# Optimization experiments

Measured on AMD Instinct MI355X. Metric: run time of the kernel, lower is better.

Reference implementation:

```python
import jax, jax.numpy as jnp
import numpy as np

B, N, D, H, DH, M = 4, 4096, 1024, 16, 64, 256
EPS = 1e-4


def softmax_kernel(data, P, is_query):
    # data: [b,h,n,dh], P: [m,dh]  (FAVOR+ positive softmax features)
    dn = data.shape[-1] ** -0.25
    ratio = P.shape[0] ** -0.5
    dd = jnp.einsum('bhnd,md->bhnm', dn * data, P)
    diag = (jnp.sum(data * data, axis=-1) * 0.5 * dn * dn)[..., None]  # [b,h,n,1]
    if is_query:
        mx = jnp.max(dd, axis=-1, keepdims=True)  # per-query max
    else:
        mx = jnp.max(dd)  # global max (as in torch source)
    return ratio * (jnp.exp(dd - diag - mx) + EPS)


def setup_inputs() -> dict:
    key = jax.random.key(0)
    ks = jax.random.split(key, 6)
    s = 1.0 / np.sqrt(D).astype(np.float32)
    x = jax.random.normal(ks[0], (B, N, D), jnp.float32)
    Wq = jax.random.normal(ks[1], (D, H * DH), jnp.float32) * s
    Wk = jax.random.normal(ks[2], (D, H * DH), jnp.float32) * s
    Wv = jax.random.normal(ks[3], (D, H * DH), jnp.float32) * s
    Wo = jax.random.normal(ks[4], (H * DH, D), jnp.float32) * s
    bo = jnp.zeros((D,), jnp.float32)
    P = jax.random.normal(ks[5], (M, DH), jnp.float32)  # gaussian (orthogonal) projection
    return {'x': x, 'Wq': Wq, 'Wk': Wk, 'Wv': Wv, 'Wo': Wo, 'bo': bo, 'P': P}


def reference(x, Wq, Wk, Wv, Wo, bo, P):
    b, n, _ = x.shape
    # qkv projections, split heads: b n (h d) -> b h n d
    def proj(W):
        return (x @ W).reshape(b, n, H, DH).transpose(0, 2, 1, 3)
    q, k, v = proj(Wq), proj(Wk), proj(Wv)
    qp = softmax_kernel(q, P, is_query=True)   # [b,h,n,m]
    kp = softmax_kernel(k, P, is_query=False)  # [b,h,n,m]
    # linear attention (Performer)
    k_cumsum = kp.sum(axis=-2)                                   # [b,h,m]
    D_inv = 1.0 / jnp.einsum('bhnm,bhm->bhn', qp, k_cumsum)      # [b,h,n]
    ctx = jnp.einsum('bhnm,bhne->bhme', kp, v)                   # [b,h,m,dh]
    out = jnp.einsum('bhme,bhnm,bhn->bhne', ctx, qp, D_inv)      # [b,h,n,dh]
    out = out.transpose(0, 2, 1, 3).reshape(b, n, H * DH)
    return out @ Wo + bo
```

## Files before the change

kernel.cpp:

```cpp
#include <hip/hip_runtime.h>
#include <math.h>

#define NB 4
#define NSEQ 4096
#define DM 1024
#define NHEAD 16
#define DHD 64
#define MF 256
#define ROWS 16384

#define DN 0.35355339059327373f
#define RATIO 0.0625f
#define HALF_DN2 0.0625f
#define EPSF 1.0e-4f

typedef __attribute__((ext_vector_type(4))) float f32x4;
typedef __attribute__((ext_vector_type(8))) short short8;
typedef __attribute__((ext_vector_type(4))) short short4v;
typedef __attribute__((ext_vector_type(8))) __bf16 bf16x8;
typedef unsigned short ushort_t;

__device__ __forceinline__ unsigned short f2bf(float f) {
  unsigned int u = __builtin_bit_cast(unsigned int, f);
  u += 0x7FFFu + ((u >> 16) & 1u);
  return (unsigned short)(u >> 16);
}
__device__ __forceinline__ float bf2f(unsigned short h) {
  unsigned int u = ((unsigned int)h) << 16;
  return __builtin_bit_cast(float, u);
}

__device__ __forceinline__ f32x4 mfma16(short8 a, short8 b, f32x4 c) {
  return __builtin_amdgcn_mfma_f32_16x16x32_bf16(
      __builtin_bit_cast(bf16x8, a), __builtin_bit_cast(bf16x8, b), c, 0, 0, 0);
}

__device__ __forceinline__ f32x4 mfma16x16(short4v a, short4v b, f32x4 c) {
#if __has_builtin(__builtin_amdgcn_mfma_f32_16x16x16bf16_1k)
  return __builtin_amdgcn_mfma_f32_16x16x16bf16_1k(a, b, c, 0, 0, 0);
#elif __has_builtin(__builtin_amdgcn_mfma_f32_16x16x16_bf16)
  typedef __attribute__((ext_vector_type(4))) __bf16 bf16x4;
  return __builtin_amdgcn_mfma_f32_16x16x16_bf16(
      __builtin_bit_cast(bf16x4, a), __builtin_bit_cast(bf16x4, b), c, 0, 0, 0);
#else
  asm volatile("s_nop 1\n\t"
               "v_mfma_f32_16x16x16_bf16 %0, %1, %2, %0\n\t"
               "s_nop 7"
               : "+v"(c) : "v"(a), "v"(b));
  return c;
#endif
}

__device__ __forceinline__ void glds16(const void* g, void* l) {
  __builtin_amdgcn_global_load_lds(
      (const __attribute__((address_space(1))) unsigned int*)g,
      (__attribute__((address_space(3))) unsigned int*)l, 16, 0, 0);
}

__global__ __launch_bounds__(256) void wtrans(const float* __restrict__ W,
                                              ushort_t* __restrict__ Wt)
{
  __shared__ float ts[64][68];
  const int tid = threadIdx.x;
  const int k0 = blockIdx.y * 64, n0 = blockIdx.x * 64;
  const int r = tid >> 4, c4 = (tid & 15) * 4;
  #pragma unroll
  for (int i = 0; i < 4; ++i) {
    float4 v = *(const float4*)&W[(size_t)(k0 + r + i * 16) * DM + n0 + c4];
    *(float4*)&ts[r + i * 16][c4] = v;
  }
  __syncthreads();
  #pragma unroll
  for (int i = 0; i < 4; ++i) {
    const int n = r + i * 16;
    ushort4 o;
    o.x = f2bf(ts[c4 + 0][n]); o.y = f2bf(ts[c4 + 1][n]);
    o.z = f2bf(ts[c4 + 2][n]); o.w = f2bf(ts[c4 + 3][n]);
    *(ushort4*)&Wt[(size_t)(n0 + n) * DM + k0 + c4] = o;
  }
}

__global__ __launch_bounds__(256) void psplit(const float* __restrict__ P,
                                              ushort_t* __restrict__ PHI,
                                              ushort_t* __restrict__ PLO)
{
  const int i = blockIdx.x * 256 + threadIdx.x;
  const float v = P[i];
  const unsigned short h = f2bf(v);
  PHI[i] = h;
  PLO[i] = f2bf(v - bf2f(h));
}

__global__ __launch_bounds__(256) void xconv(const float* __restrict__ x,
                                             ushort_t* __restrict__ xb)
{
  const size_t i = ((size_t)blockIdx.x * 256 + threadIdx.x) * 8;
  const float4 a = *(const float4*)&x[i];
  const float4 c = *(const float4*)&x[i + 4];
  short8 o;
  o[0] = f2bf(a.x); o[1] = f2bf(a.y); o[2] = f2bf(a.z); o[3] = f2bf(a.w);
  o[4] = f2bf(c.x); o[5] = f2bf(c.y); o[6] = f2bf(c.z); o[7] = f2bf(c.w);
  *(short8*)&xb[i] = o;
}

template<bool AF32, int EPI>
__global__ __launch_bounds__(256) void gemm_k(const float* __restrict__ Af,
                                              const ushort_t* __restrict__ Ab,
                                              const ushort_t* __restrict__ Bt,
                                              const float* __restrict__ bias,
                                              float* __restrict__ C,
                                              ushort_t* __restrict__ VT,
                                              ushort_t* __restrict__ OH,
                                              ushort_t* __restrict__ OL)
{
  constexpr int K = DM, N = DM;
  __shared__ ushort_t As[128 * 32];
  __shared__ ushort_t Bs[128 * 32];

  const int tid = threadIdx.x;
  const int l = tid & 63, w = tid >> 6;
  const int ll = l & 15, lh = l >> 4;
  const int wr = w >> 1, wc = w & 1;

  const int bid = blockIdx.x;
  const int swz = (bid & 7) * ((int)gridDim.x >> 3) + (bid >> 3);
  const int bm = swz >> 3, bn = swz & 7;
  const int row0 = bm * 128, col0 = bn * 128;

  const int pb0 = w * 128 + l, pb1 = pb0 + 64;
  const int brow0 = pb0 >> 2, bkq0 = (pb0 & 3) ^ ((brow0 >> 1) & 3);
  const int brow1 = pb1 >> 2, bkq1 = (pb1 & 3) ^ ((brow1 >> 1) & 3);
  const ushort_t* bsrc0 = Bt + (size_t)(col0 + brow0) * K + bkq0 * 8;
  const ushort_t* bsrc1 = Bt + (size_t)(col0 + brow1) * K + bkq1 * 8;
  ushort_t* bdst0 = &Bs[(size_t)(w * 128) * 8];
  ushort_t* bdst1 = &Bs[(size_t)(w * 128 + 64) * 8];

  const int pa0 = tid, pa1 = tid + 256;
  const int arow0 = pa0 >> 2, akq0 = (pa0 & 3) ^ ((arow0 >> 1) & 3);
  const int arow1 = pa1 >> 2, akq1 = (pa1 & 3) ^ ((arow1 >> 1) & 3);
  const float* afs0 = nullptr; const float* afs1 = nullptr;
  const ushort_t* abs0_ = nullptr; const ushort_t* abs1_ = nullptr;
  if constexpr (AF32) {
    afs0 = Af + (size_t)(row0 + arow0) * K + akq0 * 8;
    afs1 = Af + (size_t)(row0 + arow1) * K + akq1 * 8;
  } else {
    abs0_ = Ab + (size_t)(row0 + brow0) * K + bkq0 * 8;
    abs1_ = Ab + (size_t)(row0 + brow1) * K + bkq1 * 8;
  }

  int aoff[4], boff[4];
  #pragma unroll
  for (int mt = 0; mt < 4; ++mt) {
    const int r = wr * 64 + mt * 16 + ll;
    aoff[mt] = (r * 4 + (lh ^ ((r >> 1) & 3))) * 8;
  }
  #pragma unroll
  for (int nt = 0; nt < 4; ++nt) {
    const int r = wc * 64 + nt * 16 + ll;
    boff[nt] = (r * 4 + (lh ^ ((r >> 1) & 3))) * 8;
  }

  f32x4 acc[4][4];
  #pragma unroll
  for (int i = 0; i < 4; ++i)
    #pragma unroll
    for (int j = 0; j < 4; ++j) acc[i][j] = (f32x4){0.f, 0.f, 0.f, 0.f};

  for (int k0 = 0; k0 < K; k0 += 32) {
    __syncthreads();
    if constexpr (AF32) {
      const float4 u0 = *(const float4*)(afs0 + k0);
      const float4 u1 = *(const float4*)(afs0 + k0 + 4);
      const float4 v0 = *(const float4*)(afs1 + k0);
      const float4 v1 = *(const float4*)(afs1 + k0 + 4);
      short8 s0, s1;
      s0[0] = f2bf(u0.x); s0[1] = f2bf(u0.y); s0[2] = f2bf(u0.z); s0[3] = f2bf(u0.w);
      s0[4] = f2bf(u1.x); s0[5] = f2bf(u1.y); s0[6] = f2bf(u1.z); s0[7] = f2bf(u1.w);
      s1[0] = f2bf(v0.x); s1[1] = f2bf(v0.y); s1[2] = f2bf(v0.z); s1[3] = f2bf(v0.w);
      s1[4] = f2bf(v1.x); s1[5] = f2bf(v1.y); s1[6] = f2bf(v1.z); s1[7] = f2bf(v1.w);
      *(short8*)&As[(size_t)pa0 * 8] = s0;
      *(short8*)&As[(size_t)pa1 * 8] = s1;
    } else {
      glds16(abs0_ + k0, &As[(size_t)(w * 128) * 8]);
      glds16(abs1_ + k0, &As[(size_t)(w * 128 + 64) * 8]);
    }
    glds16(bsrc0 + k0, bdst0);
    glds16(bsrc1 + k0, bdst1);
    __syncthreads();

    short8 av[4], bv[4];
    #pragma unroll
    for (int mt = 0; mt < 4; ++mt) av[mt] = *(const short8*)&As[aoff[mt]];
    #pragma unroll
    for (int nt = 0; nt < 4; ++nt) bv[nt] = *(const short8*)&Bs[boff[nt]];
    #pragma unroll
    for (int mt = 0; mt < 4; ++mt)
      #pragma unroll
      for (int nt = 0; nt < 4; ++nt)
        acc[mt][nt] = mfma16(av[mt], bv[nt], acc[mt][nt]);
  }

  if constexpr (EPI <= 1) {
    #pragma unroll
    for (int mt = 0; mt < 4; ++mt) {
      #pragma unroll
      for (int nt = 0; nt < 4; ++nt) {
        const int row = row0 + wr * 64 + mt * 16 + lh * 4;
        const int col = col0 + wc * 64 + nt * 16 + ll;
        const float bv_ = (EPI == 1) ? bias[col] : 0.f;
        #pragma unroll
        for (int j = 0; j < 4; ++j)
          C[(size_t)(row + j) * N + col] = acc[mt][nt][j] + bv_;
      }
    }
  } else if constexpr (EPI == 2) {
    #pragma unroll
    for (int mt = 0; mt < 4; ++mt) {
      #pragma unroll
      for (int nt = 0; nt < 4; ++nt) {
        const int rg = row0 + wr * 64 + mt * 16 + lh * 4;
        const int cg = col0 + wc * 64 + nt * 16 + ll;
        const int b = rg >> 12, n = rg & 4095;
        const int h = cg >> 6, dh = cg & 63;
        ushort4 o;
        o.x = f2bf(acc[mt][nt][0]); o.y = f2bf(acc[mt][nt][1]);
        o.z = f2bf(acc[mt][nt][2]); o.w = f2bf(acc[mt][nt][3]);
        *(ushort4*)&VT[(((size_t)b * 16 + h) * 64 + dh) * 4096 + n] = o;
      }
    }
  } else {
    #pragma unroll
    for (int mt = 0; mt < 4; ++mt) {
      #pragma unroll
      for (int nt = 0; nt < 4; ++nt) {
        const int row = row0 + wr * 64 + mt * 16 + lh * 4;
        const int col = col0 + wc * 64 + nt * 16 + ll;
        #pragma unroll
        for (int j = 0; j < 4; ++j) {
          const float v = acc[mt][nt][j];
          const unsigned short hh = f2bf(v);
          OH[(size_t)(row + j) * N + col] = hh;
          OL[(size_t)(row + j) * N + col] = f2bf(v - bf2f(hh));
        }
      }
    }
  }
}

__global__ __launch_bounds__(256) void kmax3(const ushort_t* __restrict__ KHI,
                                             const ushort_t* __restrict__ KLO,
                                             const ushort_t* __restrict__ PHI,
                                             const ushort_t* __restrict__ PLO,
                                             unsigned* __restrict__ mxp)
{
  const int tid = threadIdx.x;
  const int l = tid & 63, mg = tid >> 6;
  const int ll = l & 15, lh = l >> 4;
  const int bh = blockIdx.x >> 4, ck = blockIdx.x & 15;
  const int b = bh >> 4, h = bh & 15;

  short8 pfh[4][2], pfl[4][2];
  #pragma unroll
  for (int mt = 0; mt < 4; ++mt)
    #pragma unroll
    for (int ks = 0; ks < 2; ++ks) {
      const size_t off = (size_t)(mg * 64 + mt * 16 + ll) * 64 + ks * 32 + lh * 8;
      pfh[mt][ks] = *(const short8*)&PHI[off];
      pfl[mt][ks] = *(const short8*)&PLO[off];
    }

  float vmax = -3.0e38f;
  for (int it = 0; it < 16; ++it) {
    const int nb = ck * 256 + it * 16;
    const size_t off = ((size_t)(b * NSEQ + nb + ll)) * DM + h * DHD + lh * 8;
    short8 kh0 = *(const short8*)&KHI[off];
    short8 kh1 = *(const short8*)&KHI[off + 32];
    short8 kl0 = *(const short8*)&KLO[off];
    short8 kl1 = *(const short8*)&KLO[off + 32];
    #pragma unroll
    for (int mt = 0; mt < 4; ++mt) {
      f32x4 acc = (f32x4){0.f, 0.f, 0.f, 0.f};
      acc = mfma16(kh0, pfh[mt][0], acc); acc = mfma16(kh1, pfh[mt][1], acc);
      acc = mfma16(kh0, pfl[mt][0], acc); acc = mfma16(kh1, pfl[mt][1], acc);
      acc = mfma16(kl0, pfh[mt][0], acc); acc = mfma16(kl1, pfh[mt][1], acc);
      vmax = fmaxf(vmax, fmaxf(fmaxf(acc[0], acc[1]), fmaxf(acc[2], acc[3])));
    }
  }
  vmax *= DN;
  #pragma unroll
  for (int off = 1; off < 64; off <<= 1) vmax = fmaxf(vmax, __shfl_xor(vmax, off, 64));
  if (l == 0) atomicMax(mxp, __float_as_uint(vmax));
}

__global__ __launch_bounds__(256) void kside4(const ushort_t* __restrict__ KHI,
                                              const ushort_t* __restrict__ KLO,
                                              const ushort_t* __restrict__ VT,
                                              const ushort_t* __restrict__ PHI,
                                              const ushort_t* __restrict__ PLO,
                                              const unsigned* __restrict__ mxp,
                                              float* __restrict__ ctx,
                                              float* __restrict__ kcs)
{
  const int tid = threadIdx.x;
  const int l = tid & 63, mg = tid >> 6;
  const int ll = l & 15, lh = l >> 4;
  const int bh = blockIdx.x >> 4, ck = blockIdx.x & 15;
  const int b = bh >> 4, h = bh & 15;

  short8 pfh[4][2], pfl[4][2];
  #pragma unroll
  for (int mt = 0; mt < 4; ++mt)
    #pragma unroll
    for (int ks = 0; ks < 2; ++ks) {
      const size_t off = (size_t)(mg * 64 + mt * 16 + ll) * 64 + ks * 32 + lh * 8;
      pfh[mt][ks] = *(const short8*)&PHI[off];
      pfl[mt][ks] = *(const short8*)&PLO[off];
    }
  const float mx = __uint_as_float(*mxp);

  f32x4 apv[4][4];
  #pragma unroll
  for (int i = 0; i < 4; ++i)
    #pragma unroll
    for (int j = 0; j < 4; ++j) apv[i][j] = (f32x4){0.f, 0.f, 0.f, 0.f};
  float kcp[4] = {0.f, 0.f, 0.f, 0.f};

  for (int it = 0; it < 16; ++it) {
    const int nb = ck * 256 + it * 16;
    const size_t off = ((size_t)(b * NSEQ + nb + ll)) * DM + h * DHD + lh * 8;
    short8 kh0 = *(const short8*)&KHI[off];
    short8 kh1 = *(const short8*)&KHI[off + 32];
    short8 kl0 = *(const short8*)&KLO[off];
    short8 kl1 = *(const short8*)&KLO[off + 32];

    float ssq = 0.f;
    #pragma unroll
    for (int e = 0; e < 8; ++e) {
      const float a0 = bf2f((ushort_t)kh0[e]) + bf2f((ushort_t)kl0[e]);
      const float a1 = bf2f((ushort_t)kh1[e]) + bf2f((ushort_t)kl1[e]);
      ssq += a0 * a0 + a1 * a1;
    }
    ssq += __shfl_xor(ssq, 16, 64);
    ssq += __shfl_xor(ssq, 32, 64);
    const float dgl = HALF_DN2 * ssq;
    float dgv[4];
    #pragma unroll
    for (int jr = 0; jr < 4; ++jr)
      dgv[jr] = __shfl(dgl, ((l >> 4) << 2) + jr, 64);

    short4v qa[4];
    #pragma unroll
    for (int mt = 0; mt < 4; ++mt) {
      f32x4 acc = (f32x4){0.f, 0.f, 0.f, 0.f};
      acc = mfma16(kh0, pfh[mt][0], acc); acc = mfma16(kh1, pfh[mt][1], acc);
      acc = mfma16(kh0, pfl[mt][0], acc); acc = mfma16(kh1, pfl[mt][1], acc);
      acc = mfma16(kl0, pfh[mt][0], acc); acc = mfma16(kl1, pfh[mt][1], acc);
      short4v o; float s = 0.f;
      #pragma unroll
      for (int jr = 0; jr < 4; ++jr) {
        const float kv = RATIO * (__expf(acc[jr] * DN - dgv[jr] - mx) + EPSF);
        const ushort_t ub = f2bf(kv);
        o[jr] = (short)ub;
        s += bf2f(ub);
      }
      qa[mt] = o;
      kcp[mt] += s;
    }
    #pragma unroll
    for (int dt = 0; dt < 4; ++dt) {
      const short4v vf = *(const short4v*)&VT[((size_t)bh * 64 + dt * 16 + ll) * NSEQ + nb + lh * 4];
      #pragma unroll
      for (int mt = 0; mt < 4; ++mt)
        apv[mt][dt] = mfma16x16(qa[mt], vf, apv[mt][dt]);
    }
  }

  #pragma unroll
  for (int mt = 0; mt < 4; ++mt) {
    float s = kcp[mt];
    s += __shfl_xor(s, 16, 64);
    s += __shfl_xor(s, 32, 64);
    if (lh == 0) atomicAdd(&kcs[bh * MF + mg * 64 + mt * 16 + ll], s);
  }
  #pragma unroll
  for (int mt = 0; mt < 4; ++mt)
    #pragma unroll
    for (int dt = 0; dt < 4; ++dt)
      #pragma unroll
      for (int jr = 0; jr < 4; ++jr) {
        const int m = mg * 64 + mt * 16 + lh * 4 + jr;
        const int dh = dt * 16 + ll;
        atomicAdd(&ctx[((size_t)bh * MF + m) * DHD + dh], apv[mt][dt][jr]);
      }
}

__global__ __launch_bounds__(256) void ctx2bf(const float* __restrict__ ctx,
                                              ushort_t* __restrict__ CTH,
                                              ushort_t* __restrict__ CTL)
{
  __shared__ float ts[64][68];
  const int tid = threadIdx.x;
  const int bh = blockIdx.x >> 2, mc = blockIdx.x & 3;
  const int r = tid >> 4, c4 = (tid & 15) * 4;
  #pragma unroll
  for (int i = 0; i < 4; ++i) {
    const int m = mc * 64 + r + i * 16;
    *(float4*)&ts[r + i * 16][c4] = *(const float4*)&ctx[((size_t)bh * MF + m) * DHD + c4];
  }
  __syncthreads();
  #pragma unroll
  for (int i = 0; i < 4; ++i) {
    const int dh = r + i * 16;
    ushort4 oh, ol;
    #pragma unroll
    for (int k = 0; k < 4; ++k) {
      const float v = ts[c4 + k][dh];
      const unsigned short hh = f2bf(v);
      ((unsigned short*)&oh)[k] = hh;
      ((unsigned short*)&ol)[k] = f2bf(v - bf2f(hh));
    }
    const size_t o = ((size_t)bh * 64 + dh) * MF + mc * 64 + c4;
    *(ushort4*)&CTH[o] = oh;
    *(ushort4*)&CTL[o] = ol;
  }
}

__global__ __launch_bounds__(512, 2) void qside5(const ushort_t* __restrict__ QHI,
                                                 const ushort_t* __restrict__ QLO,
                                                 const ushort_t* __restrict__ PHI,
                                                 const ushort_t* __restrict__ PLO,
                                                 const float* __restrict__ kcs,
                                                 const ushort_t* __restrict__ CTH,
                                                 const ushort_t* __restrict__ CTL,
                                                 ushort_t* __restrict__ attb)
{
  extern __shared__ ushort_t lds[];
  ushort_t* pst = lds;
  ushort_t* ctf = lds + 32768;
  ushort_t* kcf = lds + 65536;

  const int tid = threadIdx.x;
  const int l = tid & 63, w = tid >> 6;
  const int ll = l & 15, lh = l >> 4;
  const int bh = blockIdx.x >> 4, qt = blockIdx.x & 15;
  const int b = bh >> 4, h = bh & 15;

  #pragma unroll
  for (int i = 0; i < 8; ++i) {
    const int f = tid + i * 512;
    const int fl = f & 63, r = f >> 6;
    const int p = r & 1, ks = (r >> 1) & 1, mt = r >> 2;
    const ushort_t* src = (p ? PLO : PHI) + (mt * 16 + (fl & 15)) * 64 + ks * 32 + (fl >> 4) * 8;
    *(short8*)&pst[f * 8] = *(const short8*)src;
  }
  #pragma unroll
  for (int i = 0; i < 16; ++i) {
    const int g = tid + i * 512;
    const int gl = g & 63, r = g >> 6;
    const int dt = r & 3, r2 = r >> 2, mt = r2 & 15, p = r2 >> 4;
    const ushort_t* src = (p ? CTL : CTH) +
        ((size_t)bh * 64 + dt * 16 + (gl & 15)) * MF + mt * 16 + (gl >> 4) * 4;
    *(ushort4*)&ctf[g * 4] = *(const ushort4*)src;
  }
  #pragma unroll
  for (int i = 0; i < 2; ++i) {
    const int u = tid + i * 512;
    const int ul = u & 63, mt = u >> 6;
    const int cll = ul & 15, clh = ul >> 4;
    ushort4 o = make_ushort4(0, 0, 0, 0);
    if (cll < 2) {
      #pragma unroll
      for (int e = 0; e < 4; ++e) {
        const float kv = kcs[bh * MF + mt * 16 + clh * 4 + e];
        const unsigned short hi = f2bf(kv);
        ((ushort_t*)&o)[e] = (cll == 0) ? hi : f2bf(kv - bf2f(hi));
      }
    }
    *(ushort4*)&kcf[u * 4] = o;
  }
  __syncthreads();

  const int rowb0 = b * NSEQ + qt * 256 + w * 32;

  short8 qh0[2], ql0[2], qh1[2], ql1[2];
  #pragma unroll
  for (int ks = 0; ks < 2; ++ks) {
    const size_t off = (size_t)(rowb0 + ll) * DM + h * DHD + ks * 32 + lh * 8;
    qh0[ks] = *(const short8*)&QHI[off];
    ql0[ks] = *(const short8*)&QLO[off];
    qh1[ks] = *(const short8*)&QHI[off + (size_t)16 * DM];
    ql1[ks] = *(const short8*)&QLO[off + (size_t)16 * DM];
  }
  float ssq0 = 0.f, ssq1 = 0.f;
  #pragma unroll
  for (int ks = 0; ks < 2; ++ks)
    #pragma unroll
    for (int e = 0; e < 8; ++e) {
      const float a0 = bf2f((ushort_t)qh0[ks][e]) + bf2f((ushort_t)ql0[ks][e]);
      const float a1 = bf2f((ushort_t)qh1[ks][e]) + bf2f((ushort_t)ql1[ks][e]);
      ssq0 += a0 * a0; ssq1 += a1 * a1;
    }
  ssq0 += __shfl_xor(ssq0, 16, 64); ssq0 += __shfl_xor(ssq0, 32, 64);
  ssq1 += __shfl_xor(ssq1, 16, 64); ssq1 += __shfl_xor(ssq1, 32, 64);
  const float dg0 = HALF_DN2 * ssq0, dg1 = HALF_DN2 * ssq1;

  f32x4 dd0[16], dd1[16];
  #pragma unroll
  for (int mt = 0; mt < 16; ++mt) {
    const short8 ph0 = *(const short8*)&pst[((mt * 2 + 0) * 2 + 0) * 512 + l * 8];
    const short8 ph1 = *(const short8*)&pst[((mt * 2 + 1) * 2 + 0) * 512 + l * 8];
    const short8 pl0 = *(const short8*)&pst[((mt * 2 + 0) * 2 + 1) * 512 + l * 8];
    const short8 pl1 = *(const short8*)&pst[((mt * 2 + 1) * 2 + 1) * 512 + l * 8];
    f32x4 a0 = (f32x4){0.f, 0.f, 0.f, 0.f};
    f32x4 a1 = (f32x4){0.f, 0.f, 0.f, 0.f};
    a0 = mfma16(ph0, qh0[0], a0); a0 = mfma16(ph1, qh0[1], a0);
    a0 = mfma16(ph0, ql0[0], a0); a0 = mfma16(ph1, ql0[1], a0);
    a0 = mfma16(pl0, qh0[0], a0); a0 = mfma16(pl1, qh0[1], a0);
    a1 = mfma16(ph0, qh1[0], a1); a1 = mfma16(ph1, qh1[1], a1);
    a1 = mfma16(ph0, ql1[0], a1); a1 = mfma16(ph1, ql1[1], a1);
    a1 = mfma16(pl0, qh1[0], a1); a1 = mfma16(pl1, qh1[1], a1);
    dd0[mt] = a0; dd1[mt] = a1;
  }

  float rm0 = -3.0e38f, rm1 = -3.0e38f;
  #pragma unroll
  for (int mt = 0; mt < 16; ++mt) {
    rm0 = fmaxf(rm0, fmaxf(fmaxf(dd0[mt][0], dd0[mt][1]), fmaxf(dd0[mt][2], dd0[mt][3])));
    rm1 = fmaxf(rm1, fmaxf(fmaxf(dd1[mt][0], dd1[mt][1]), fmaxf(dd1[mt][2], dd1[mt][3])));
  }
  rm0 = fmaxf(rm0, __shfl_xor(rm0, 16, 64)); rm0 = fmaxf(rm0, __shfl_xor(rm0, 32, 64));
  rm1 = fmaxf(rm1, __shfl_xor(rm1, 16, 64)); rm1 = fmaxf(rm1, __shfl_xor(rm1, 32, 64));
  rm0 *= DN; rm1 *= DN;

  short4v qp0[16], qp1[16];
  #pragma unroll
  for (int mt = 0; mt < 16; ++mt) {
    short4v o0, o1;
    #pragma unroll
    for (int jr = 0; jr < 4; ++jr) {
      o0[jr] = (short)f2bf(RATIO * (__expf(dd0[mt][jr] * DN - dg0 - rm0) + EPSF));
      o1[jr] = (short)f2bf(RATIO * (__expf(dd1[mt][jr] * DN - dg1 - rm1) + EPSF));
    }
    qp0[mt] = o0; qp1[mt] = o1;
  }

  f32x4 av0[4], av1[4];
  #pragma unroll
  for (int dt = 0; dt < 4; ++dt) {
    av0[dt] = (f32x4){0.f, 0.f, 0.f, 0.f};
    av1[dt] = (f32x4){0.f, 0.f, 0.f, 0.f};
  }
  f32x4 aK0 = (f32x4){0.f, 0.f, 0.f, 0.f};
  f32x4 aK1 = (f32x4){0.f, 0.f, 0.f, 0.f};
  #pragma unroll
  for (int mt = 0; mt < 16; ++mt) {
    const short4v kcv = *(const short4v*)&kcf[mt * 256 + l * 4];
    aK0 = mfma16x16(qp0[mt], kcv, aK0);
    aK1 = mfma16x16(qp1[mt], kcv, aK1);
    #pragma unroll
    for (int dt = 0; dt < 4; ++dt) {
      const short4v ch = *(const short4v*)&ctf[((0 * 16 + mt) * 4 + dt) * 256 + l * 4];
      const short4v cl = *(const short4v*)&ctf[((16 + mt) * 4 + dt) * 256 + l * 4];
      av0[dt] = mfma16x16(qp0[mt], ch, av0[dt]);
      av0[dt] = mfma16x16(qp0[mt], cl, av0[dt]);
      av1[dt] = mfma16x16(qp1[mt], ch, av1[dt]);
      av1[dt] = mfma16x16(qp1[mt], cl, av1[dt]);
    }
  }

  float di0[4], di1[4];
  #pragma unroll
  for (int jr = 0; jr < 4; ++jr) {
    const float h0 = __shfl(aK0[jr], (l & 48), 64);
    const float l0 = __shfl(aK0[jr], (l & 48) | 1, 64);
    const float h1 = __shfl(aK1[jr], (l & 48), 64);
    const float l1 = __shfl(aK1[jr], (l & 48) | 1, 64);
    di0[jr] = 1.0f / (h0 + l0);
    di1[jr] = 1.0f / (h1 + l1);
  }

  #pragma unroll
  for (int dt = 0; dt < 4; ++dt)
    #pragma unroll
    for (int jr = 0; jr < 4; ++jr) {
      const int col = h * DHD + dt * 16 + ll;
      attb[(size_t)(rowb0 + lh * 4 + jr) * DM + col] = f2bf(av0[dt][jr] * di0[jr]);
      attb[(size_t)(rowb0 + 16 + lh * 4 + jr) * DM + col] = f2bf(av1[dt][jr] * di1[jr]);
    }
}

extern "C" void kernel_launch(void* const* d_in, const int* in_sizes, int n_in,
                              void* d_out, int out_size, void* d_ws, size_t ws_size,
                              hipStream_t stream)
{
  const float* x  = (const float*)d_in[0];
  const float* Wq = (const float*)d_in[1];
  const float* Wk = (const float*)d_in[2];
  const float* Wv = (const float*)d_in[3];
  const float* Wo = (const float*)d_in[4];
  const float* bo = (const float*)d_in[5];
  const float* P  = (const float*)d_in[6];
  float* out = (float*)d_out;

  char* wp = (char*)d_ws;
  ushort_t* QHI = (ushort_t*)(wp + 0);
  ushort_t* QLO = (ushort_t*)(wp + 33554432);
  ushort_t* KHI = (ushort_t*)(wp + 67108864);
  ushort_t* KLO = (ushort_t*)(wp + 100663296);
  ushort_t* VT  = (ushort_t*)(wp + 134217728);
  ushort_t* Wqt = (ushort_t*)(wp + 167772160);
  ushort_t* Wkt = (ushort_t*)(wp + 169869312);
  ushort_t* Wvt = (ushort_t*)(wp + 171966464);
  ushort_t* Wot = (ushort_t*)(wp + 174063616);
  ushort_t* PHI = (ushort_t*)(wp + 176160768);
  ushort_t* PLO = (ushort_t*)(wp + 176193536);
  float*    CTX = (float*)(wp + 176226304);
  float*    KCS = (float*)(wp + 180420608);
  unsigned* MX  = (unsigned*)(wp + 180486144);
  ushort_t* CTH = (ushort_t*)(wp + 180486400);
  ushort_t* CTL = (ushort_t*)(wp + 182583552);
  ushort_t* XB  = (ushort_t*)(wp + 184680704);
  ushort_t* ATTB = KHI;

  const bool useXB = ws_size >= 218235136ull;

  dim3 tg(16, 16);
  wtrans<<<tg, 256, 0, stream>>>(Wq, Wqt);
  wtrans<<<tg, 256, 0, stream>>>(Wk, Wkt);
  wtrans<<<tg, 256, 0, stream>>>(Wv, Wvt);
  wtrans<<<tg, 256, 0, stream>>>(Wo, Wot);
  psplit<<<64, 256, 0, stream>>>(P, PHI, PLO);

  if (useXB) {
    xconv<<<8192, 256, 0, stream>>>(x, XB);
    gemm_k<false, 3><<<1024, 256, 0, stream>>>(nullptr, XB, Wqt, nullptr, nullptr, nullptr, QHI, QLO);
    gemm_k<false, 3><<<1024, 256, 0, stream>>>(nullptr, XB, Wkt, nullptr, nullptr, nullptr, KHI, KLO);
    gemm_k<false, 2><<<1024, 256, 0, stream>>>(nullptr, XB, Wvt, nullptr, nullptr, VT, nullptr, nullptr);
  } else {
    gemm_k<true, 3><<<1024, 256, 0, stream>>>(x, nullptr, Wqt, nullptr, nullptr, nullptr, QHI, QLO);
    gemm_k<true, 3><<<1024, 256, 0, stream>>>(x, nullptr, Wkt, nullptr, nullptr, nullptr, KHI, KLO);
    gemm_k<true, 2><<<1024, 256, 0, stream>>>(x, nullptr, Wvt, nullptr, nullptr, VT, nullptr, nullptr);
  }

  hipMemsetAsync(CTX, 0, 4194304 + 65536 + 256, stream);

  kmax3<<<1024, 256, 0, stream>>>(KHI, KLO, PHI, PLO, MX);
  kside4<<<1024, 256, 0, stream>>>(KHI, KLO, VT, PHI, PLO, MX, CTX, KCS);
  ctx2bf<<<256, 256, 0, stream>>>(CTX, CTH, CTL);
  qside5<<<1024, 512, 139264, stream>>>(QHI, QLO, PHI, PLO, KCS, CTH, CTL, ATTB);

  gemm_k<false, 1><<<1024, 256, 0, stream>>>(nullptr, ATTB, Wot, bo, out, nullptr, nullptr, nullptr);
}
```

Baseline: 534.5 us.

## Fuse key max pass into key-side accumulation with online rescaling

Replaces the separate key-max kernel and atomic-based key-side kernel with one pass that keeps a running per-wave max with deferred rescaling. It writes per-chunk partial context and key sums that a combine kernel later rescales by the global max, and folds the epsilon term in through a V column sum. The projection GEMM epilogue now computes the squared-norm diagonal and writes interleaved hi/lo Q/K rows. Scratch buffers live in the output buffer so the bf16 x path is always taken. This removes one full read of K, the fp32 atomics and the extra memset, at the cost of larger partial buffers and a more complex combine step.

```diff
diff --git a/kernel.cpp b/kernel.cpp
--- a/kernel.cpp
+++ b/kernel.cpp
@@ -13,6 +13,7 @@
 #define RATIO 0.0625f
 #define HALF_DN2 0.0625f
 #define EPSF 1.0e-4f
+#define THR_DEFER 4.0f
 
 typedef __attribute__((ext_vector_type(4))) float f32x4;
 typedef __attribute__((ext_vector_type(8))) short short8;
@@ -103,15 +104,14 @@
   *(short8*)&xb[i] = o;
 }
 
-template<bool AF32, int EPI>
-__global__ __launch_bounds__(256) void gemm_k(const float* __restrict__ Af,
-                                              const ushort_t* __restrict__ Ab,
+template<int EPI>
+__global__ __launch_bounds__(256) void gemm_k(const ushort_t* __restrict__ Ab,
                                               const ushort_t* __restrict__ Bt,
                                               const float* __restrict__ bias,
                                               float* __restrict__ C,
                                               ushort_t* __restrict__ VT,
-                                              ushort_t* __restrict__ OH,
-                                              ushort_t* __restrict__ OL)
+                                              ushort_t* __restrict__ OHL,
+                                              float* __restrict__ DIAG)
 {
   constexpr int K = DM, N = DM;
   __shared__ ushort_t As[128 * 32];
@@ -135,18 +135,8 @@
   ushort_t* bdst0 = &Bs[(size_t)(w * 128) * 8];
   ushort_t* bdst1 = &Bs[(size_t)(w * 128 + 64) * 8];
 
-  const int pa0 = tid, pa1 = tid + 256;
-  const int arow0 = pa0 >> 2, akq0 = (pa0 & 3) ^ ((arow0 >> 1) & 3);
-  const int arow1 = pa1 >> 2, akq1 = (pa1 & 3) ^ ((arow1 >> 1) & 3);
-  const float* afs0 = nullptr; const float* afs1 = nullptr;
-  const ushort_t* abs0_ = nullptr; const ushort_t* abs1_ = nullptr;
-  if constexpr (AF32) {
-    afs0 = Af + (size_t)(row0 + arow0) * K + akq0 * 8;
-    afs1 = Af + (size_t)(row0 + arow1) * K + akq1 * 8;
-  } else {
-    abs0_ = Ab + (size_t)(row0 + brow0) * K + bkq0 * 8;
-    abs1_ = Ab + (size_t)(row0 + brow1) * K + bkq1 * 8;
-  }
+  const ushort_t* asrc0 = Ab + (size_t)(row0 + brow0) * K + bkq0 * 8;
+  const ushort_t* asrc1 = Ab + (size_t)(row0 + brow1) * K + bkq1 * 8;
 
   int aoff[4], boff[4];
   #pragma unroll
@@ -168,22 +158,8 @@
 
   for (int k0 = 0; k0 < K; k0 += 32) {
     __syncthreads();
-    if constexpr (AF32) {
-      const float4 u0 = *(const float4*)(afs0 + k0);
-      const float4 u1 = *(const float4*)(afs0 + k0 + 4);
-      const float4 v0 = *(const float4*)(afs1 + k0);
-      const float4 v1 = *(const float4*)(afs1 + k0 + 4);
-      short8 s0, s1;
-      s0[0] = f2bf(u0.x); s0[1] = f2bf(u0.y); s0[2] = f2bf(u0.z); s0[3] = f2bf(u0.w);
-      s0[4] = f2bf(u1.x); s0[5] = f2bf(u1.y); s0[6] = f2bf(u1.z); s0[7] = f2bf(u1.w);
-      s1[0] = f2bf(v0.x); s1[1] = f2bf(v0.y); s1[2] = f2bf(v0.z); s1[3] = f2bf(v0.w);
-      s1[4] = f2bf(v1.x); s1[5] = f2bf(v1.y); s1[6] = f2bf(v1.z); s1[7] = f2bf(v1.w);
-      *(short8*)&As[(size_t)pa0 * 8] = s0;
-      *(short8*)&As[(size_t)pa1 * 8] = s1;
-    } else {
-      glds16(abs0_ + k0, &As[(size_t)(w * 128) * 8]);
-      glds16(abs1_ + k0, &As[(size_t)(w * 128 + 64) * 8]);
-    }
+    glds16(asrc0 + k0, &As[(size_t)(w * 128) * 8]);
+    glds16(asrc1 + k0, &As[(size_t)(w * 128 + 64) * 8]);
     glds16(bsrc0 + k0, bdst0);
     glds16(bsrc1 + k0, bdst1);
     __syncthreads();
@@ -200,14 +176,14 @@
         acc[mt][nt] = mfma16(av[mt], bv[nt], acc[mt][nt]);
   }
 
-  if constexpr (EPI <= 1) {
+  if constexpr (EPI == 1) {
     #pragma unroll
     for (int mt = 0; mt < 4; ++mt) {
       #pragma unroll
       for (int nt = 0; nt < 4; ++nt) {
         const int row = row0 + wr * 64 + mt * 16 + lh * 4;
         const int col = col0 + wc * 64 + nt * 16 + ll;
-        const float bv_ = (EPI == 1) ? bias[col] : 0.f;
+        const float bv_ = bias[col];
         #pragma unroll
         for (int j = 0; j < 4; ++j)
           C[(size_t)(row + j) * N + col] = acc[mt][nt][j] + bv_;
@@ -229,34 +205,54 @@
       }
     }
   } else {
+    const int hglob = (col0 >> 6) + wc;
     #pragma unroll
     for (int mt = 0; mt < 4; ++mt) {
+      float rssq[4] = {0.f, 0.f, 0.f, 0.f};
       #pragma unroll
       for (int nt = 0; nt < 4; ++nt) {
         const int row = row0 + wr * 64 + mt * 16 + lh * 4;
-        const int col = col0 + wc * 64 + nt * 16 + ll;
+        const int e = nt * 16 + ll;
         #pragma unroll
         for (int j = 0; j < 4; ++j) {
           const float v = acc[mt][nt][j];
+          rssq[j] += v * v;
           const unsigned short hh = f2bf(v);
-          OH[(size_t)(row + j) * N + col] = hh;
-          OL[(size_t)(row + j) * N + col] = f2bf(v - bf2f(hh));
+          const size_t base = ((size_t)(row + j) * 16 + hglob) * 128 + e;
+          OHL[base] = hh;
+          OHL[base + 64] = f2bf(v - bf2f(hh));
         }
       }
-    }
-  }
-}
-
-__global__ __launch_bounds__(256) void kmax3(const ushort_t* __restrict__ KHI,
-                                             const ushort_t* __restrict__ KLO,
-                                             const ushort_t* __restrict__ PHI,
-                                             const ushort_t* __restrict__ PLO,
-                                             unsigned* __restrict__ mxp)
+      #pragma unroll
+      for (int j = 0; j < 4; ++j) {
+        float s = rssq[j];
+        s += __shfl_xor(s, 1, 64); s += __shfl_xor(s, 2, 64);
+        s += __shfl_xor(s, 4, 64); s += __shfl_xor(s, 8, 64);
+        if (ll == 0) {
+          const int row = row0 + wr * 64 + mt * 16 + lh * 4 + j;
+          DIAG[(((row >> 12) * 16 + hglob) << 12) + (row & 4095)] = HALF_DN2 * s;
+        }
+      }
+    }
+  }
+}
+
+__global__ __launch_bounds__(256) void kside5(const ushort_t* __restrict__ KHL,
+                                              const ushort_t* __restrict__ VT,
+                                              const ushort_t* __restrict__ PHI,
+                                              const ushort_t* __restrict__ PLO,
+                                              const float* __restrict__ DIAGK,
+                                              float* __restrict__ partC,
+                                              float* __restrict__ partK,
+                                              float* __restrict__ mw,
+                                              float* __restrict__ vsum,
+                                              unsigned* __restrict__ mxp)
 {
   const int tid = threadIdx.x;
   const int l = tid & 63, mg = tid >> 6;
   const int ll = l & 15, lh = l >> 4;
-  const int bh = blockIdx.x >> 4, ck = blockIdx.x & 15;
+  const int blk = blockIdx.x;
+  const int bh = blk >> 3, ck = blk & 7;
   const int b = bh >> 4, h = bh & 15;
 
   short8 pfh[4][2], pfl[4][2];
@@ -269,110 +265,104 @@
       pfl[mt][ks] = *(const short8*)&PLO[off];
     }
 
-  float vmax = -3.0e38f;
-  for (int it = 0; it < 16; ++it) {
-    const int nb = ck * 256 + it * 16;
-    const size_t off = ((size_t)(b * NSEQ + nb + ll)) * DM + h * DHD + lh * 8;
-    short8 kh0 = *(const short8*)&KHI[off];
-    short8 kh1 = *(const short8*)&KHI[off + 32];
-    short8 kl0 = *(const short8*)&KLO[off];
-    short8 kl1 = *(const short8*)&KLO[off + 32];
+  f32x4 apv[4][4];
+  #pragma unroll
+  for (int i = 0; i < 4; ++i)
+    #pragma unroll
+    for (int j = 0; j < 4; ++j) apv[i][j] = (f32x4){0.f, 0.f, 0.f, 0.f};
+  float kcp[4] = {0.f, 0.f, 0.f, 0.f};
+  float vs[4] = {0.f, 0.f, 0.f, 0.f};
+  float m_run = -1.0e30f, tmax = -1.0e30f;
+
+  const int n0 = ck * 512;
+  const ushort_t* krow = KHL + ((size_t)(b * NSEQ + n0 + ll) * 16 + h) * 128 + lh * 8;
+  const ushort_t* vrow = VT + (size_t)bh * 64 * NSEQ + n0 + lh * 4;
+  const float* drow = DIAGK + bh * 4096 + n0 + lh * 4;
+
+  short8 kh0 = *(const short8*)(krow);
+  short8 kh1 = *(const short8*)(krow + 32);
+  short8 kl0 = *(const short8*)(krow + 64);
+  short8 kl1 = *(const short8*)(krow + 96);
+
+  for (int it = 0; it < 32; ++it) {
+    short8 nh0, nh1, nl0, nl1;
+    if (it < 31) {
+      const ushort_t* kp = krow + (size_t)(it + 1) * 16 * 2048;
+      nh0 = *(const short8*)(kp);
+      nh1 = *(const short8*)(kp + 32);
+      nl0 = *(const short8*)(kp + 64);
+      nl1 = *(const short8*)(kp + 96);
+    }
+    const float4 dg4 = *(const float4*)(drow + it * 16);
+    short4v vf[4];
+    #pragma unroll
+    for (int dt = 0; dt < 4; ++dt)
+      vf[dt] = *(const short4v*)&vrow[(size_t)(dt * 16 + ll) * NSEQ + it * 16];
+
+    f32x4 dda[4];
     #pragma unroll
     for (int mt = 0; mt < 4; ++mt) {
       f32x4 acc = (f32x4){0.f, 0.f, 0.f, 0.f};
       acc = mfma16(kh0, pfh[mt][0], acc); acc = mfma16(kh1, pfh[mt][1], acc);
       acc = mfma16(kh0, pfl[mt][0], acc); acc = mfma16(kh1, pfl[mt][1], acc);
       acc = mfma16(kl0, pfh[mt][0], acc); acc = mfma16(kl1, pfh[mt][1], acc);
-      vmax = fmaxf(vmax, fmaxf(fmaxf(acc[0], acc[1]), fmaxf(acc[2], acc[3])));
-    }
-  }
-  vmax *= DN;
-  #pragma unroll
-  for (int off = 1; off < 64; off <<= 1) vmax = fmaxf(vmax, __shfl_xor(vmax, off, 64));
-  if (l == 0) atomicMax(mxp, __float_as_uint(vmax));
-}
-
-__global__ __launch_bounds__(256) void kside4(const ushort_t* __restrict__ KHI,
-                                              const ushort_t* __restrict__ KLO,
-                                              const ushort_t* __restrict__ VT,
-                                              const ushort_t* __restrict__ PHI,
-                                              const ushort_t* __restrict__ PLO,
-                                              const unsigned* __restrict__ mxp,
-                                              float* __restrict__ ctx,
-                                              float* __restrict__ kcs)
-{
-  const int tid = threadIdx.x;
-  const int l = tid & 63, mg = tid >> 6;
-  const int ll = l & 15, lh = l >> 4;
-  const int bh = blockIdx.x >> 4, ck = blockIdx.x & 15;
-  const int b = bh >> 4, h = bh & 15;
-
-  short8 pfh[4][2], pfl[4][2];
-  #pragma unroll
-  for (int mt = 0; mt < 4; ++mt)
-    #pragma unroll
-    for (int ks = 0; ks < 2; ++ks) {
-      const size_t off = (size_t)(mg * 64 + mt * 16 + ll) * 64 + ks * 32 + lh * 8;
-      pfh[mt][ks] = *(const short8*)&PHI[off];
-      pfl[mt][ks] = *(const short8*)&PLO[off];
-    }
-  const float mx = __uint_as_float(*mxp);
-
-  f32x4 apv[4][4];
-  #pragma unroll
-  for (int i = 0; i < 4; ++i)
-    #pragma unroll
-    for (int j = 0; j < 4; ++j) apv[i][j] = (f32x4){0.f, 0.f, 0.f, 0.f};
-  float kcp[4] = {0.f, 0.f, 0.f, 0.f};
-
-  for (int it = 0; it < 16; ++it) {
-    const int nb = ck * 256 + it * 16;
-    const size_t off = ((size_t)(b * NSEQ + nb + ll)) * DM + h * DHD + lh * 8;
-    short8 kh0 = *(const short8*)&KHI[off];
-    short8 kh1 = *(const short8*)&KHI[off + 32];
-    short8 kl0 = *(const short8*)&KLO[off];
-    short8 kl1 = *(const short8*)&KLO[off + 32];
-
-    float ssq = 0.f;
-    #pragma unroll
-    for (int e = 0; e < 8; ++e) {
-      const float a0 = bf2f((ushort_t)kh0[e]) + bf2f((ushort_t)kl0[e]);
-      const float a1 = bf2f((ushort_t)kh1[e]) + bf2f((ushort_t)kl1[e]);
-      ssq += a0 * a0 + a1 * a1;
-    }
-    ssq += __shfl_xor(ssq, 16, 64);
-    ssq += __shfl_xor(ssq, 32, 64);
-    const float dgl = HALF_DN2 * ssq;
-    float dgv[4];
-    #pragma unroll
-    for (int jr = 0; jr < 4; ++jr)
-      dgv[jr] = __shfl(dgl, ((l >> 4) << 2) + jr, 64);
-
+      #pragma unroll
+      for (int jr = 0; jr < 4; ++jr) acc[jr] *= DN;
+      dda[mt] = acc;
+    }
+
+    float pm = -1.0e30f;
+    #pragma unroll
+    for (int mt = 0; mt < 4; ++mt)
+      #pragma unroll
+      for (int jr = 0; jr < 4; ++jr) pm = fmaxf(pm, dda[mt][jr]);
+    tmax = fmaxf(tmax, pm);
+    if (!__all(pm <= m_run + THR_DEFER)) {
+      float pw = pm;
+      pw = fmaxf(pw, __shfl_xor(pw, 1, 64));  pw = fmaxf(pw, __shfl_xor(pw, 2, 64));
+      pw = fmaxf(pw, __shfl_xor(pw, 4, 64));  pw = fmaxf(pw, __shfl_xor(pw, 8, 64));
+      pw = fmaxf(pw, __shfl_xor(pw, 16, 64)); pw = fmaxf(pw, __shfl_xor(pw, 32, 64));
+      const float sc = __expf(m_run - pw);
+      #pragma unroll
+      for (int mt = 0; mt < 4; ++mt) {
+        kcp[mt] *= sc;
+        #pragma unroll
+        for (int dt = 0; dt < 4; ++dt) apv[mt][dt] *= sc;
+      }
+      m_run = pw;
+    }
+
+    const float dgv[4] = {dg4.x, dg4.y, dg4.z, dg4.w};
     short4v qa[4];
     #pragma unroll
     for (int mt = 0; mt < 4; ++mt) {
-      f32x4 acc = (f32x4){0.f, 0.f, 0.f, 0.f};
-      acc = mfma16(kh0, pfh[mt][0], acc); acc = mfma16(kh1, pfh[mt][1], acc);
-      acc = mfma16(kh0, pfl[mt][0], acc); acc = mfma16(kh1, pfl[mt][1], acc);
-      acc = mfma16(kl0, pfh[mt][0], acc); acc = mfma16(kl1, pfh[mt][1], acc);
-      short4v o; float s = 0.f;
+      short4v o;
+      float s = 0.f;
       #pragma unroll
       for (int jr = 0; jr < 4; ++jr) {
-        const float kv = RATIO * (__expf(acc[jr] * DN - dgv[jr] - mx) + EPSF);
-        const ushort_t ub = f2bf(kv);
+        const float kv = __expf(dda[mt][jr] - dgv[jr] - m_run);
+        const unsigned short ub = f2bf(kv);
         o[jr] = (short)ub;
         s += bf2f(ub);
       }
       qa[mt] = o;
       kcp[mt] += s;
     }
-    #pragma unroll
-    for (int dt = 0; dt < 4; ++dt) {
-      const short4v vf = *(const short4v*)&VT[((size_t)bh * 64 + dt * 16 + ll) * NSEQ + nb + lh * 4];
+
+    if (mg == 0) {
+      #pragma unroll
+      for (int dt = 0; dt < 4; ++dt)
+        #pragma unroll
+        for (int e = 0; e < 4; ++e) vs[dt] += bf2f((ushort_t)vf[dt][e]);
+    }
+
+    #pragma unroll
+    for (int dt = 0; dt < 4; ++dt)
       #pragma unroll
       for (int mt = 0; mt < 4; ++mt)
-        apv[mt][dt] = mfma16x16(qa[mt], vf, apv[mt][dt]);
-    }
+        apv[mt][dt] = mfma16x16(qa[mt], vf[dt], apv[mt][dt]);
+
+    kh0 = nh0; kh1 = nh1; kl0 = nl0; kl1 = nl1;
   }
 
   #pragma unroll
@@ -380,7 +370,7 @@
     float s = kcp[mt];
     s += __shfl_xor(s, 16, 64);
     s += __shfl_xor(s, 32, 64);
-    if (lh == 0) atomicAdd(&kcs[bh * MF + mg * 64 + mt * 16 + ll], s);
+    if (lh == 0) partK[blk * 256 + mg * 64 + mt * 16 + ll] = s;
   }
   #pragma unroll
   for (int mt = 0; mt < 4; ++mt)
@@ -390,22 +380,66 @@
       for (int jr = 0; jr < 4; ++jr) {
         const int m = mg * 64 + mt * 16 + lh * 4 + jr;
         const int dh = dt * 16 + ll;
-        atomicAdd(&ctx[((size_t)bh * MF + m) * DHD + dh], apv[mt][dt][jr]);
-      }
-}
-
-__global__ __launch_bounds__(256) void ctx2bf(const float* __restrict__ ctx,
-                                              ushort_t* __restrict__ CTH,
-                                              ushort_t* __restrict__ CTL)
-{
-  __shared__ float ts[64][68];
+        partC[(size_t)blk * 16384 + (size_t)m * 64 + dh] = apv[mt][dt][jr];
+      }
+  if (mg == 0) {
+    #pragma unroll
+    for (int dt = 0; dt < 4; ++dt) {
+      float s = vs[dt];
+      s += __shfl_xor(s, 16, 64);
+      s += __shfl_xor(s, 32, 64);
+      if (lh == 0) atomicAdd(&vsum[bh * 64 + dt * 16 + ll], s);
+    }
+  }
+  tmax = fmaxf(tmax, __shfl_xor(tmax, 1, 64));  tmax = fmaxf(tmax, __shfl_xor(tmax, 2, 64));
+  tmax = fmaxf(tmax, __shfl_xor(tmax, 4, 64));  tmax = fmaxf(tmax, __shfl_xor(tmax, 8, 64));
+  tmax = fmaxf(tmax, __shfl_xor(tmax, 16, 64)); tmax = fmaxf(tmax, __shfl_xor(tmax, 32, 64));
+  if (l == 0) {
+    atomicMax(mxp, __float_as_uint(tmax));
+    mw[blk * 4 + mg] = m_run;
+  }
+}
+
+__global__ __launch_bounds__(256) void combine(const float* __restrict__ partC,
+                                               const float* __restrict__ partK,
+                                               const float* __restrict__ mw,
+                                               const float* __restrict__ vsum,
+                                               const unsigned* __restrict__ mxp,
+                                               float* __restrict__ KCS,
+                                               ushort_t* __restrict__ CTH,
+                                               ushort_t* __restrict__ CTL)
+{
   const int tid = threadIdx.x;
   const int bh = blockIdx.x >> 2, mc = blockIdx.x & 3;
+  const float MX = __uint_as_float(*mxp);
+  float s[8];
+  #pragma unroll
+  for (int c = 0; c < 8; ++c)
+    s[c] = RATIO * __expf(mw[(bh * 8 + c) * 4 + mc] - MX);
+
+  __shared__ float ts[64][68];
   const int r = tid >> 4, c4 = (tid & 15) * 4;
+  const float reps = RATIO * EPSF;
+  const float4 v4 = *(const float4*)&vsum[bh * 64 + c4];
   #pragma unroll
   for (int i = 0; i < 4; ++i) {
-    const int m = mc * 64 + r + i * 16;
-    *(float4*)&ts[r + i * 16][c4] = *(const float4*)&ctx[((size_t)bh * MF + m) * DHD + c4];
+    const int ml = r + i * 16;
+    float4 a;
+    a.x = reps * v4.x; a.y = reps * v4.y; a.z = reps * v4.z; a.w = reps * v4.w;
+    #pragma unroll
+    for (int c = 0; c < 8; ++c) {
+      const float4 p = *(const float4*)&partC[(size_t)(bh * 8 + c) * 16384 +
+                                              (size_t)(mc * 64 + ml) * 64 + c4];
+      a.x += s[c] * p.x; a.y += s[c] * p.y; a.z += s[c] * p.z; a.w += s[c] * p.w;
+    }
+    *(float4*)&ts[ml][c4] = a;
+  }
+  if (tid < 64) {
+    const int m = mc * 64 + tid;
+    float kv = reps * 4096.0f;
+    #pragma unroll
+    for (int c = 0; c < 8; ++c) kv += s[c] * partK[(bh * 8 + c) * 256 + m];
+    KCS[bh * 256 + m] = kv;
   }
   __syncthreads();
   #pragma unroll
@@ -425,10 +459,10 @@
   }
 }
 
-__global__ __launch_bounds__(512, 2) void qside5(const ushort_t* __restrict__ QHI,
-                                                 const ushort_t* __restrict__ QLO,
+__global__ __launch_bounds__(512, 2) void qside6(const ushort_t* __restrict__ QHL,
                                                  const ushort_t* __restrict__ PHI,
                                                  const ushort_t* __restrict__ PLO,
+                                                 const float* __restrict__ DIAGQ,
                                                  const float* __restrict__ kcs,
                                                  const ushort_t* __restrict__ CTH,
                                                  const ushort_t* __restrict__ CTL,
@@ -480,29 +514,20 @@
   }
   __syncthreads();
 
-  const int rowb0 = b * NSEQ + qt * 256 + w * 32;
+  const int nloc0 = qt * 256 + w * 32;
+  const int rowb0 = b * NSEQ + nloc0;
 
   short8 qh0[2], ql0[2], qh1[2], ql1[2];
   #pragma unroll
   for (int ks = 0; ks < 2; ++ks) {
-    const size_t off = (size_t)(rowb0 + ll) * DM + h * DHD + ks * 32 + lh * 8;
-    qh0[ks] = *(const short8*)&QHI[off];
-    ql0[ks] = *(const short8*)&QLO[off];
-    qh1[ks] = *(const short8*)&QHI[off + (size_t)16 * DM];
-    ql1[ks] = *(const short8*)&QLO[off + (size_t)16 * DM];
-  }
-  float ssq0 = 0.f, ssq1 = 0.f;
-  #pragma unroll
-  for (int ks = 0; ks < 2; ++ks)
-    #pragma unroll
-    for (int e = 0; e < 8; ++e) {
-      const float a0 = bf2f((ushort_t)qh0[ks][e]) + bf2f((ushort_t)ql0[ks][e]);
-      const float a1 = bf2f((ushort_t)qh1[ks][e]) + bf2f((ushort_t)ql1[ks][e]);
-      ssq0 += a0 * a0; ssq1 += a1 * a1;
-    }
-  ssq0 += __shfl_xor(ssq0, 16, 64); ssq0 += __shfl_xor(ssq0, 32, 64);
-  ssq1 += __shfl_xor(ssq1, 16, 64); ssq1 += __shfl_xor(ssq1, 32, 64);
-  const float dg0 = HALF_DN2 * ssq0, dg1 = HALF_DN2 * ssq1;
+    const size_t base = ((size_t)(rowb0 + ll) * 16 + h) * 128 + ks * 32 + lh * 8;
+    qh0[ks] = *(const short8*)&QHL[base];
+    ql0[ks] = *(const short8*)&QHL[base + 64];
+    qh1[ks] = *(const short8*)&QHL[base + (size_t)16 * 2048];
+    ql1[ks] = *(const short8*)&QHL[base + (size_t)16 * 2048 + 64];
+  }
+  const float dg0 = DIAGQ[bh * 4096 + nloc0 + ll];
+  const float dg1 = DIAGQ[bh * 4096 + nloc0 + 16 + ll];
 
   f32x4 dd0[16], dd1[16];
   #pragma unroll
@@ -603,26 +628,28 @@
   float* out = (float*)d_out;
 
   char* wp = (char*)d_ws;
-  ushort_t* QHI = (ushort_t*)(wp + 0);
-  ushort_t* QLO = (ushort_t*)(wp + 33554432);
-  ushort_t* KHI = (ushort_t*)(wp + 67108864);
-  ushort_t* KLO = (ushort_t*)(wp + 100663296);
-  ushort_t* VT  = (ushort_t*)(wp + 134217728);
-  ushort_t* Wqt = (ushort_t*)(wp + 167772160);
-  ushort_t* Wkt = (ushort_t*)(wp + 169869312);
-  ushort_t* Wvt = (ushort_t*)(wp + 171966464);
-  ushort_t* Wot = (ushort_t*)(wp + 174063616);
-  ushort_t* PHI = (ushort_t*)(wp + 176160768);
-  ushort_t* PLO = (ushort_t*)(wp + 176193536);
-  float*    CTX = (float*)(wp + 176226304);
-  float*    KCS = (float*)(wp + 180420608);
-  unsigned* MX  = (unsigned*)(wp + 180486144);
-  ushort_t* CTH = (ushort_t*)(wp + 180486400);
-  ushort_t* CTL = (ushort_t*)(wp + 182583552);
-  ushort_t* XB  = (ushort_t*)(wp + 184680704);
-  ushort_t* ATTB = KHI;
-
-  const bool useXB = ws_size >= 218235136ull;
+  ushort_t* QHL  = (ushort_t*)(wp + 0);
+  ushort_t* KHL  = (ushort_t*)(wp + 67108864);
+  ushort_t* VT   = (ushort_t*)(wp + 134217728);
+  ushort_t* Wqt  = (ushort_t*)(wp + 167772160);
+  ushort_t* Wkt  = (ushort_t*)(wp + 169869312);
+  ushort_t* Wvt  = (ushort_t*)(wp + 171966464);
+  ushort_t* Wot  = (ushort_t*)(wp + 174063616);
+  ushort_t* PHI  = (ushort_t*)(wp + 176160768);
+  ushort_t* PLO  = (ushort_t*)(wp + 176193536);
+  float*    DIAGQ= (float*)(wp + 176226304);
+  float*    DIAGK= (float*)(wp + 177274880);
+  float*    PARTK= (float*)(wp + 178323456);
+  float*    MW   = (float*)(wp + 178847744);
+  float*    VSUM = (float*)(wp + 178855936);
+  unsigned* MX   = (unsigned*)(wp + 178872320);
+  float*    KCS  = (float*)(wp + 178872576);
+  ushort_t* CTH  = (ushort_t*)(wp + 178938112);
+  ushort_t* CTL  = (ushort_t*)(wp + 181035264);
+  ushort_t* ATTB = KHL;
+
+  float*    PARTC= (float*)d_out;
+  ushort_t* XB   = (ushort_t*)((char*)d_out + 33554432);
 
   dim3 tg(16, 16);
   wtrans<<<tg, 256, 0, stream>>>(Wq, Wqt);
@@ -630,24 +657,16 @@
   wtrans<<<tg, 256, 0, stream>>>(Wv, Wvt);
   wtrans<<<tg, 256, 0, stream>>>(Wo, Wot);
   psplit<<<64, 256, 0, stream>>>(P, PHI, PLO);
-
-  if (useXB) {
-    xconv<<<8192, 256, 0, stream>>>(x, XB);
-    gemm_k<false, 3><<<1024, 256, 0, stream>>>(nullptr, XB, Wqt, nullptr, nullptr, nullptr, QHI, QLO);
-    gemm_k<false, 3><<<1024, 256, 0, stream>>>(nullptr, XB, Wkt, nullptr, nullptr, nullptr, KHI, KLO);
-    gemm_k<false, 2><<<1024, 256, 0, stream>>>(nullptr, XB, Wvt, nullptr, nullptr, VT, nullptr, nullptr);
-  } else {
-    gemm_k<true, 3><<<1024, 256, 0, stream>>>(x, nullptr, Wqt, nullptr, nullptr, nullptr, QHI, QLO);
-    gemm_k<true, 3><<<1024, 256, 0, stream>>>(x, nullptr, Wkt, nullptr, nullptr, nullptr, KHI, KLO);
-    gemm_k<true, 2><<<1024, 256, 0, stream>>>(x, nullptr, Wvt, nullptr, nullptr, VT, nullptr, nullptr);
-  }
-
-  hipMemsetAsync(CTX, 0, 4194304 + 65536 + 256, stream);
-
-  kmax3<<<1024, 256, 0, stream>>>(KHI, KLO, PHI, PLO, MX);
-  kside4<<<1024, 256, 0, stream>>>(KHI, KLO, VT, PHI, PLO, MX, CTX, KCS);
-  ctx2bf<<<256, 256, 0, stream>>>(CTX, CTH, CTL);
-  qside5<<<1024, 512, 139264, stream>>>(QHI, QLO, PHI, PLO, KCS, CTH, CTL, ATTB);
-
-  gemm_k<false, 1><<<1024, 256, 0, stream>>>(nullptr, ATTB, Wot, bo, out, nullptr, nullptr, nullptr);
-}
+  xconv<<<8192, 256, 0, stream>>>(x, XB);
+  hipMemsetAsync(VSUM, 0, 16384 + 256, stream);
+
+  gemm_k<3><<<1024, 256, 0, stream>>>(XB, Wqt, nullptr, nullptr, nullptr, QHL, DIAGQ);
+  gemm_k<3><<<1024, 256, 0, stream>>>(XB, Wkt, nullptr, nullptr, nullptr, KHL, DIAGK);
+  gemm_k<2><<<1024, 256, 0, stream>>>(XB, Wvt, nullptr, nullptr, VT, nullptr, nullptr);
+
+  kside5<<<512, 256, 0, stream>>>(KHL, VT, PHI, PLO, DIAGK, PARTC, PARTK, MW, VSUM, MX);
+  combine<<<256, 256, 0, stream>>>(PARTC, PARTK, MW, VSUM, MX, KCS, CTH, CTL);
+  qside6<<<1024, 512, 139264, stream>>>(QHL, PHI, PLO, DIAGQ, KCS, CTH, CTL, ATTB);
+
+  gemm_k<1><<<1024, 256, 0, stream>>>(ATTB, Wot, bo, out, nullptr, nullptr, nullptr);
+}
```

Result: faster. 427.6 us (-20.0%).
